# Performance work log

Measured on AMD Instinct MI355X. Metric: run time of the kernel, lower is better.

Reference implementation:

```python
import jax, jax.numpy as jnp
import numpy as np

EMBED_DIM = 512
NUM_HEADS = 8
HEAD_DIM = EMBED_DIM // NUM_HEADS
FACTOR = 5
B, T = 4, 2048


def setup_inputs() -> dict:
    key = jax.random.key(0)
    ks = jax.random.split(key, 10)
    s = EMBED_DIM ** -0.5
    hidden_states = jax.random.normal(ks[0], (B, T, EMBED_DIM), dtype=jnp.float32)
    log_L = int(np.ceil(np.log1p(T)))
    u_part = min(FACTOR * T * log_L, T)
    index_sample = jax.random.randint(ks[1], (u_part,), 0, T, dtype=jnp.int32)
    Wq = jax.random.normal(ks[2], (EMBED_DIM, EMBED_DIM), dtype=jnp.float32) * s
    bq = jnp.zeros((EMBED_DIM,), dtype=jnp.float32)
    Wk = jax.random.normal(ks[3], (EMBED_DIM, EMBED_DIM), dtype=jnp.float32) * s
    bk = jnp.zeros((EMBED_DIM,), dtype=jnp.float32)
    Wv = jax.random.normal(ks[4], (EMBED_DIM, EMBED_DIM), dtype=jnp.float32) * s
    bv = jnp.zeros((EMBED_DIM,), dtype=jnp.float32)
    Wo = jax.random.normal(ks[5], (EMBED_DIM, EMBED_DIM), dtype=jnp.float32) * s
    bo = jnp.zeros((EMBED_DIM,), dtype=jnp.float32)
    return {"hidden_states": hidden_states, "index_sample": index_sample,
            "Wq": Wq, "bq": bq, "Wk": Wk, "bk": bk, "Wv": Wv, "bv": bv,
            "Wo": Wo, "bo": bo}


def _split_heads(x, bsz, seqlen):
    # [B, T, E] -> [B*H, T, head_dim]
    return x.reshape(bsz, seqlen, NUM_HEADS, HEAD_DIM).transpose(0, 2, 1, 3).reshape(bsz * NUM_HEADS, seqlen, HEAD_DIM)


def reference(hidden_states, index_sample, Wq, bq, Wk, bk, Wv, bv, Wo, bo):
    bsz, tgt_len, embed_dim = hidden_states.shape
    scaling = HEAD_DIM ** -0.5
    q = (hidden_states @ Wq.T + bq) * scaling
    k = hidden_states @ Wk.T + bk
    v = hidden_states @ Wv.T + bv
    q = _split_heads(q, bsz, tgt_len)   # [BH, T, d]
    k = _split_heads(k, bsz, tgt_len)
    v = _split_heads(v, bsz, tgt_len)
    L_k = tgt_len
    log_q = int(np.ceil(np.log1p(tgt_len)))
    u = min(FACTOR * log_q, tgt_len)
    # random key sampling (indices precomputed, length u_part)
    k_sample = k[:, index_sample, :]                                  # [BH, u_part, d]
    qk_sample = jnp.einsum('bqd,bkd->bqk', q, k_sample)               # [BH, T, u_part]
    # sparsity measurement: max - mean over sampled keys (mean uses full L_k as in source)
    sparsity = qk_sample.max(axis=-1) - qk_sample.sum(axis=-1) / L_k  # [BH, T]
    top_idx = jax.lax.top_k(sparsity, u)[1]                           # [BH, u]
    q_reduce = jnp.take_along_axis(q, top_idx[:, :, None], axis=1)    # [BH, u, d]
    attn = jax.nn.softmax(jnp.einsum('bud,bkd->buk', q_reduce, k), axis=-1)  # [BH, u, L]
    attn_out = jnp.einsum('buk,bkd->bud', attn, v)                    # [BH, u, d]
    # encoder context: mean of values over time, scattered with active-query outputs
    context = jnp.broadcast_to(v.mean(axis=1, keepdims=True), v.shape)  # [BH, T, d]
    bh_idx = jnp.arange(bsz * NUM_HEADS)[:, None]
    context = context.at[bh_idx, top_idx].set(attn_out)
    out = context.reshape(bsz, NUM_HEADS, tgt_len, HEAD_DIM).transpose(0, 2, 1, 3).reshape(bsz, tgt_len, embed_dim)
    return out @ Wo.T + bo
```

## Files before the change

kernel.cpp:

```cpp
#include <hip/hip_runtime.h>
#include <hip/hip_bf16.h>
#include <math.h>

#define T_LEN 2048
#define EMB   512
#define NHEAD 8
#define HDIM  64
#define BHEADS 32
#define USEL  40

typedef __bf16 bf16v8 __attribute__((ext_vector_type(8)));
typedef _Float16 f16x8 __attribute__((ext_vector_type(8)));
typedef float f32x4 __attribute__((ext_vector_type(4)));
typedef unsigned short u16;

__device__ __forceinline__ void cvt4_hilo(const float4 f, uint2& ph, uint2& pl)
{
    __hip_bfloat16 h0 = __float2bfloat16(f.x);
    __hip_bfloat16 h1 = __float2bfloat16(f.y);
    __hip_bfloat16 h2 = __float2bfloat16(f.z);
    __hip_bfloat16 h3 = __float2bfloat16(f.w);
    __hip_bfloat16 l0 = __float2bfloat16(f.x - __bfloat162float(h0));
    __hip_bfloat16 l1 = __float2bfloat16(f.y - __bfloat162float(h1));
    __hip_bfloat16 l2 = __float2bfloat16(f.z - __bfloat162float(h2));
    __hip_bfloat16 l3 = __float2bfloat16(f.w - __bfloat162float(h3));
    ph.x = (unsigned)*(const u16*)&h0 | ((unsigned)*(const u16*)&h1 << 16);
    ph.y = (unsigned)*(const u16*)&h2 | ((unsigned)*(const u16*)&h3 << 16);
    pl.x = (unsigned)*(const u16*)&l0 | ((unsigned)*(const u16*)&l1 << 16);
    pl.y = (unsigned)*(const u16*)&l2 | ((unsigned)*(const u16*)&l3 << 16);
}

__device__ __forceinline__ void cvt4_hilo_h(const float4 f, uint2& ph, uint2& pl)
{
    _Float16 h0 = (_Float16)f.x;
    _Float16 h1 = (_Float16)f.y;
    _Float16 h2 = (_Float16)f.z;
    _Float16 h3 = (_Float16)f.w;
    _Float16 l0 = (_Float16)(f.x - (float)h0);
    _Float16 l1 = (_Float16)(f.y - (float)h1);
    _Float16 l2 = (_Float16)(f.z - (float)h2);
    _Float16 l3 = (_Float16)(f.w - (float)h3);
    ph.x = (unsigned)*(const u16*)&h0 | ((unsigned)*(const u16*)&h1 << 16);
    ph.y = (unsigned)*(const u16*)&h2 | ((unsigned)*(const u16*)&h3 << 16);
    pl.x = (unsigned)*(const u16*)&l0 | ((unsigned)*(const u16*)&l1 << 16);
    pl.y = (unsigned)*(const u16*)&l2 | ((unsigned)*(const u16*)&l3 << 16);
}

__global__ __launch_bounds__(256)
void pack_hilo_kernel(const float* __restrict__ X,
                      const float* __restrict__ Wq, const float* __restrict__ Wk,
                      const float* __restrict__ Wv,
                      u16* __restrict__ Xp, u16* __restrict__ Wp)
{
    alignas(16) __shared__ u16 th[4096];
    alignas(16) __shared__ u16 tl[4096];
    const int b = blockIdx.x, tid = threadIdx.x;

    const float* src; u16* dst;
    if (b < 1024) {
        int mt = b >> 4, kt = b & 15;
        src = X + (size_t)(mt * 128) * EMB + kt * 32;
        dst = Xp + (size_t)b * 8192;
    } else {
        int wdx = b - 1024;
        int z = wdx >> 6, nt = (wdx >> 4) & 3, kt = wdx & 15;
        const float* W = (z == 0) ? Wq : (z == 1) ? Wk : Wv;
        src = W + (size_t)(nt * 128) * EMB + kt * 32;
        dst = Wp + (size_t)wdx * 8192;
    }

    #pragma unroll
    for (int s = 0; s < 4; ++s) {
        int u = tid + 256 * s;
        int row = u >> 3, c4 = u & 7;
        float4 f = *(const float4*)&src[(size_t)row * EMB + c4 * 4];
        uint2 ph, pl;
        cvt4_hilo_h(f, ph, pl);
        int kq = c4 >> 1, e4 = (c4 & 1) * 4;
        *(uint2*)&th[kq * 1024 + row * 8 + e4] = ph;
        *(uint2*)&tl[kq * 1024 + row * 8 + e4] = pl;
    }
    __syncthreads();

    uint4* d4 = (uint4*)dst;
    const uint4* s4h = (const uint4*)th;
    const uint4* s4l = (const uint4*)tl;
    d4[tid]       = s4h[tid];
    d4[tid + 256] = s4h[tid + 256];
    d4[tid + 512] = s4l[tid];
    d4[tid + 768] = s4l[tid + 256];
}

__global__ __launch_bounds__(256)
void qkv_mfma_kernel(const u16* __restrict__ Xp, const u16* __restrict__ Wp,
                     const float* __restrict__ bq, const float* __restrict__ bk,
                     const float* __restrict__ bv,
                     float* __restrict__ qo, float* __restrict__ ko, float* __restrict__ vo)
{
    alignas(16) __shared__ u16 Ah[4096];
    alignas(16) __shared__ u16 Al[4096];
    alignas(16) __shared__ u16 Bh[4096];
    alignas(16) __shared__ u16 Bl[4096];

    const int z = blockIdx.z;
    const float* bias; float* dst; float scale;
    if (z == 0)      { bias = bq; dst = qo; scale = 0.125f; }
    else if (z == 1) { bias = bk; dst = ko; scale = 1.0f;   }
    else             { bias = bv; dst = vo; scale = 1.0f;   }
    const bool three = (z != 2);

    const int tid = threadIdx.x;
    const int mt = blockIdx.x;
    const int nt = blockIdx.y;
    const int w = tid >> 6, lane = tid & 63;
    const int wm = w & 1, wn = w >> 1;
    const int lm = lane & 15, kq = lane >> 4;

    const u16* Abase = Xp + (size_t)mt * (16 * 8192);
    const u16* Bbase = Wp + (size_t)(z * 4 + nt) * (16 * 8192);

    f32x4 acc[4][4];
    #pragma unroll
    for (int i = 0; i < 4; ++i)
        #pragma unroll
        for (int j = 0; j < 4; ++j)
            #pragma unroll
            for (int r = 0; r < 4; ++r) acc[i][j][r] = 0.0f;

    for (int kt = 0; kt < 16; ++kt) {
        __syncthreads();
        const u16* at = Abase + kt * 8192;
        const u16* bt = Bbase + kt * 8192;
        const u16* gsrc; u16* ldst;
        if (w == 0)      { gsrc = at;        ldst = Ah; }
        else if (w == 1) { gsrc = at + 4096; ldst = Al; }
        else if (w == 2) { gsrc = bt;        ldst = Bh; }
        else             { gsrc = bt + 4096; ldst = Bl; }
        if (three || (w & 1) == 0) {
            #pragma unroll
            for (int i = 0; i < 8; ++i)
                __builtin_amdgcn_global_load_lds(
                    (const __attribute__((address_space(1))) void*)(gsrc + (size_t)lane * 8 + i * 512),
                    (__attribute__((address_space(3))) void*)(ldst + i * 512),
                    16, 0, 0);
        }
        __syncthreads();

        f16x8 ah[4], al[4], bh[4], bl[4];
        #pragma unroll
        for (int i = 0; i < 4; ++i) {
            int ar = (wm * 64 + i * 16 + lm) * 8 + kq * 1024;
            int br = (wn * 64 + i * 16 + lm) * 8 + kq * 1024;
            ah[i] = *(const f16x8*)&Ah[ar];
            bh[i] = *(const f16x8*)&Bh[br];
            if (three) {
                al[i] = *(const f16x8*)&Al[ar];
                bl[i] = *(const f16x8*)&Bl[br];
            }
        }
        #pragma unroll
        for (int i = 0; i < 4; ++i)
            #pragma unroll
            for (int j = 0; j < 4; ++j) {
                acc[i][j] = __builtin_amdgcn_mfma_f32_16x16x32_f16(ah[i], bh[j], acc[i][j], 0, 0, 0);
                if (three) {
                    acc[i][j] = __builtin_amdgcn_mfma_f32_16x16x32_f16(ah[i], bl[j], acc[i][j], 0, 0, 0);
                    acc[i][j] = __builtin_amdgcn_mfma_f32_16x16x32_f16(al[i], bh[j], acc[i][j], 0, 0, 0);
                }
            }
    }

    #pragma unroll
    for (int j = 0; j < 4; ++j) {
        int ng = nt * 128 + wn * 64 + j * 16 + lm;
        int h = ng >> 6, d = ng & 63;
        float bv_ = bias[ng];
        #pragma unroll
        for (int i = 0; i < 4; ++i) {
            #pragma unroll
            for (int r = 0; r < 4; ++r) {
                int mg = mt * 128 + wm * 64 + i * 16 + kq * 4 + r;
                int b = mg >> 11, t = mg & 2047;
                dst[((size_t)((b * NHEAD + h) * T_LEN + t)) * HDIM + d] =
                    (acc[i][j][r] + bv_) * scale;
            }
        }
    }
}

__global__ __launch_bounds__(256)
void qkv_proj_kernel(const float* __restrict__ X,
                     const float* __restrict__ Wq, const float* __restrict__ bq,
                     const float* __restrict__ Wk, const float* __restrict__ bk,
                     const float* __restrict__ Wv, const float* __restrict__ bv,
                     float* __restrict__ qo, float* __restrict__ ko, float* __restrict__ vo)
{
    alignas(16) __shared__ u16 Ah[128 * 40];
    alignas(16) __shared__ u16 Al[128 * 40];
    alignas(16) __shared__ u16 Bh[128 * 40];
    alignas(16) __shared__ u16 Bl[128 * 40];

    const int z = blockIdx.z;
    const float* W; const float* bias; float* dst; float scale;
    if (z == 0)      { W = Wq; bias = bq; dst = qo; scale = 0.125f; }
    else if (z == 1) { W = Wk; bias = bk; dst = ko; scale = 1.0f;   }
    else             { W = Wv; bias = bv; dst = vo; scale = 1.0f;   }

    const int tid = threadIdx.x;
    const int m0 = blockIdx.x * 128;
    const int n0 = blockIdx.y * 128;
    const int w = tid >> 6, lane = tid & 63;
    const int wm = w & 1, wn = w >> 1;
    const int lm = lane & 15, kq = lane >> 4;

    f32x4 acc[4][4];
    #pragma unroll
    for (int i = 0; i < 4; ++i)
        #pragma unroll
        for (int j = 0; j < 4; ++j)
            #pragma unroll
            for (int r = 0; r < 4; ++r) acc[i][j][r] = 0.0f;

    for (int kc = 0; kc < EMB; kc += 32) {
        __syncthreads();
        #pragma unroll
        for (int s = 0; s < 4; ++s) {
            int u = tid + 256 * s;
            int row = u >> 3, c4 = u & 7;
            float4 fa = *(const float4*)&X[(size_t)(m0 + row) * EMB + kc + c4 * 4];
            float4 fb = *(const float4*)&W[(n0 + row) * EMB + kc + c4 * 4];
            uint2 ph, pl;
            cvt4_hilo_h(fa, ph, pl);
            *(uint2*)&Ah[row * 40 + c4 * 4] = ph;
            *(uint2*)&Al[row * 40 + c4 * 4] = pl;
            cvt4_hilo_h(fb, ph, pl);
            *(uint2*)&Bh[row * 40 + c4 * 4] = ph;
            *(uint2*)&Bl[row * 40 + c4 * 4] = pl;
        }
        __syncthreads();

        f16x8 ah[4], al[4], bh[4], bl[4];
        #pragma unroll
        for (int i = 0; i < 4; ++i) {
            int ra = (wm * 64 + i * 16 + lm) * 40 + kq * 8;
            ah[i] = *(const f16x8*)&Ah[ra];
            al[i] = *(const f16x8*)&Al[ra];
            int rb = (wn * 64 + i * 16 + lm) * 40 + kq * 8;
            bh[i] = *(const f16x8*)&Bh[rb];
            bl[i] = *(const f16x8*)&Bl[rb];
        }
        #pragma unroll
        for (int i = 0; i < 4; ++i)
            #pragma unroll
            for (int j = 0; j < 4; ++j) {
                acc[i][j] = __builtin_amdgcn_mfma_f32_16x16x32_f16(ah[i], bh[j], acc[i][j], 0, 0, 0);
                acc[i][j] = __builtin_amdgcn_mfma_f32_16x16x32_f16(ah[i], bl[j], acc[i][j], 0, 0, 0);
                acc[i][j] = __builtin_amdgcn_mfma_f32_16x16x32_f16(al[i], bh[j], acc[i][j], 0, 0, 0);
            }
    }

    #pragma unroll
    for (int j = 0; j < 4; ++j) {
        int ng = n0 + wn * 64 + j * 16 + lm;
        int h = ng >> 6, d = ng & 63;
        float bv_ = bias[ng];
        #pragma unroll
        for (int i = 0; i < 4; ++i) {
            #pragma unroll
            for (int r = 0; r < 4; ++r) {
                int mg = m0 + wm * 64 + i * 16 + kq * 4 + r;
                int b = mg >> 11, t = mg & 2047;
                dst[((size_t)((b * NHEAD + h) * T_LEN + t)) * HDIM + d] =
                    (acc[i][j][r] + bv_) * scale;
            }
        }
    }
}

__global__ __launch_bounds__(256)
void count_compact_kernel(const int* __restrict__ idxs, int n,
                          int* __restrict__ count, int* __restrict__ klist,
                          int* __restrict__ ncp)
{
    __shared__ int cnt[T_LEN];
    __shared__ int th_tot[256];
    __shared__ int th_off[256];
    __shared__ int ncs;
    const int tid = threadIdx.x;
    for (int j = tid; j < T_LEN; j += 256) cnt[j] = 0;
    __syncthreads();
    for (int i = tid; i < n; i += 256) atomicAdd(&cnt[idxs[i] & (T_LEN - 1)], 1);
    __syncthreads();
    const int base = tid * 8;
    int flags[8]; int loc = 0;
    #pragma unroll
    for (int j = 0; j < 8; ++j) {
        int c = cnt[base + j];
        count[base + j] = c;
        flags[j] = (c > 0); loc += flags[j];
    }
    th_tot[tid] = loc;
    __syncthreads();
    if (tid == 0) {
        int run = 0;
        for (int i = 0; i < 256; ++i) { th_off[i] = run; run += th_tot[i]; }
        ncs = run;
        ncp[0] = run;
    }
    __syncthreads();
    int off = th_off[tid];
    #pragma unroll
    for (int j = 0; j < 8; ++j)
        if (flags[j]) klist[off++] = base + j;
    __syncthreads();
    const int nc = ncs;
    const int nt = (nc + 127) & ~127;
    const int k0 = klist[0];
    for (int j = nc + tid; j < nt; j += 256) klist[j] = k0;
}

__global__ __launch_bounds__(256)
void ksum_vmean_part_kernel(const int* __restrict__ count,
                            const float* __restrict__ k, const float* __restrict__ v,
                            float* __restrict__ kpart, float* __restrict__ vpart)
{
    __shared__ int cs[256];
    alignas(16) __shared__ float rk[16 * 64];
    alignas(16) __shared__ float rv[16 * 64];

    const int sl = blockIdx.x, bh = blockIdx.y, tid = threadIdx.x;
    const int f4 = tid & 15, tg = tid >> 4;
    const int t0 = sl * 256;

    cs[tid] = count[t0 + tid];
    __syncthreads();

    const float4* k4 = (const float4*)(k + (size_t)bh * T_LEN * HDIM) + t0 * 16;
    const float4* v4 = (const float4*)(v + (size_t)bh * T_LEN * HDIM) + t0 * 16;

    float4 ak = {0.f, 0.f, 0.f, 0.f}, av = {0.f, 0.f, 0.f, 0.f};
    #pragma unroll
    for (int s = 0; s < 16; ++s) {
        int t = tg + s * 16;
        float c = (float)cs[t];
        float4 kf = k4[t * 16 + f4];
        float4 vf = v4[t * 16 + f4];
        ak.x = fmaf(c, kf.x, ak.x); ak.y = fmaf(c, kf.y, ak.y);
        ak.z = fmaf(c, kf.z, ak.z); ak.w = fmaf(c, kf.w, ak.w);
        av.x += vf.x; av.y += vf.y; av.z += vf.z; av.w += vf.w;
    }
    *(float4*)&rk[tg * 64 + f4 * 4] = ak;
    *(float4*)&rv[tg * 64 + f4 * 4] = av;
    __syncthreads();

    if (tid < 64) {
        float sk = 0.f, sv = 0.f;
        #pragma unroll
        for (int g = 0; g < 16; ++g) { sk += rk[g * 64 + tid]; sv += rv[g * 64 + tid]; }
        kpart[((size_t)bh * 8 + sl) * 64 + tid] = sk;
        vpart[((size_t)bh * 8 + sl) * 64 + tid] = sv;
    }
}

__global__ __launch_bounds__(64)
void ksum_vmean_reduce_kernel(const float* __restrict__ kpart, const float* __restrict__ vpart,
                              float* __restrict__ ksum, float* __restrict__ vmean)
{
    const int bh = blockIdx.x, d = threadIdx.x;
    float sk = 0.f, sv = 0.f;
    #pragma unroll
    for (int sl = 0; sl < 8; ++sl) {
        sk += kpart[((size_t)bh * 8 + sl) * 64 + d];
        sv += vpart[((size_t)bh * 8 + sl) * 64 + d];
    }
    ksum[bh * 64 + d]  = sk;
    vmean[bh * 64 + d] = sv * (1.0f / 2048.0f);
}

__global__ __launch_bounds__(256)
void pack_k_kernel(const float* __restrict__ k, const int* __restrict__ klist,
                   const int* __restrict__ ncp, u16* __restrict__ Kp)
{
    alignas(16) __shared__ u16 th[8192];
    alignas(16) __shared__ u16 tl[8192];
    const int wg = blockIdx.x, tid = threadIdx.x;
    const int swz = (wg & 7) * 64 + (wg >> 3);
    const int bh = swz >> 4, kt = swz & 15;
    const int ntiles = (ncp[0] + 127) >> 7;
    if (kt >= ntiles) return;

    const float4* kb4 = (const float4*)(k + (size_t)bh * T_LEN * HDIM);
    #pragma unroll
    for (int s = 0; s < 8; ++s) {
        int u = tid + 256 * s;
        int row = u >> 4, c4 = u & 15;
        int krow = klist[kt * 128 + row];
        float4 f = kb4[krow * 16 + c4];
        uint2 ph, pl;
        cvt4_hilo_h(f, ph, pl);
        int base = (c4 >> 3) * 4096 + ((c4 >> 1) & 3) * 1024 + row * 8 + (c4 & 1) * 4;
        *(uint2*)&th[base] = ph;
        *(uint2*)&tl[base] = pl;
    }
    __syncthreads();

    u16* dst = Kp + ((size_t)bh * 16 + kt) * 16384;
    uint4* d4 = (uint4*)dst;
    const uint4* s4h = (const uint4*)th;
    const uint4* s4l = (const uint4*)tl;
    #pragma unroll
    for (int i = 0; i < 4; ++i) d4[tid + 256 * i] = s4h[tid + 256 * i];
    #pragma unroll
    for (int i = 0; i < 4; ++i) d4[1024 + tid + 256 * i] = s4l[tid + 256 * i];
}

__global__ __launch_bounds__(256)
void sparsity_scan_kernel(const float* __restrict__ q, const u16* __restrict__ Kp,
                          const float* __restrict__ ksum,
                          const int* __restrict__ ncp, float* __restrict__ spars)
{
    alignas(16) __shared__ u16 KH[10240];
    alignas(16) __shared__ u16 KL[10240];
    __shared__ float ksm[64];
    __shared__ float smax[128];
    __shared__ float sdotL[128];

    const int tid = threadIdx.x;
    const int wg = blockIdx.x;
    const int swz = (wg & 7) * 64 + (wg >> 3);
    const int bh = swz >> 4;
    const int q0 = (swz & 15) * 128;
    const int w = tid >> 6, lane = tid & 63;
    const int lm = lane & 15, kq = lane >> 4;

    const float* qb = q + ((size_t)bh * T_LEN + q0) * HDIM;
    const int ntiles = (ncp[0] + 127) >> 7;

    if (tid < 64) ksm[tid] = ksum[bh * 64 + tid];

    #pragma unroll
    for (int s = 0; s < 8; ++s) {
        int u = tid + 256 * s;
        int row = u >> 4, c4 = u & 15;
        float4 f = *(const float4*)&qb[row * HDIM + c4 * 4];
        uint2 ph, pl;
        cvt4_hilo_h(f, ph, pl);
        int base = ((c4 >> 3) * 128 + row) * 40 + (c4 & 7) * 4;
        *(uint2*)&KH[base] = ph;
        *(uint2*)&KL[base] = pl;
    }
    __syncthreads();

    f16x8 qh[2][2], ql[2][2];
    #pragma unroll
    for (int i = 0; i < 2; ++i)
        #pragma unroll
        for (int c = 0; c < 2; ++c) {
            int ra = (c * 128 + w * 32 + i * 16 + lm) * 40 + kq * 8;
            qh[i][c] = *(const f16x8*)&KH[ra];
            ql[i][c] = *(const f16x8*)&KL[ra];
        }

    {
        float4 k0a = *(const float4*)&ksm[kq * 8];
        float4 k0b = *(const float4*)&ksm[kq * 8 + 4];
        float4 k1a = *(const float4*)&ksm[32 + kq * 8];
        float4 k1b = *(const float4*)&ksm[32 + kq * 8 + 4];
        float kmv[2][8] = {{k0a.x, k0a.y, k0a.z, k0a.w, k0b.x, k0b.y, k0b.z, k0b.w},
                           {k1a.x, k1a.y, k1a.z, k1a.w, k1b.x, k1b.y, k1b.z, k1b.w}};
        #pragma unroll
        for (int i = 0; i < 2; ++i) {
            float sd = 0.f;
            #pragma unroll
            for (int c = 0; c < 2; ++c)
                #pragma unroll
                for (int e = 0; e < 8; ++e)
                    sd = fmaf((float)qh[i][c][e] + (float)ql[i][c][e], kmv[c][e], sd);
            sd += __shfl_xor(sd, 16, 64);
            sd += __shfl_xor(sd, 32, 64);
            if (kq == 0) sdotL[w * 32 + i * 16 + lm] = sd;
        }
    }

    float vmax[2][4];
    #pragma unroll
    for (int i = 0; i < 2; ++i)
        #pragma unroll
        for (int r = 0; r < 4; ++r) vmax[i][r] = -INFINITY;

    const u16* kpb = Kp + (size_t)bh * (16 * 16384);

    for (int kt = 0; kt < ntiles; ++kt) {
        __syncthreads();
        const u16* kp = kpb + kt * 16384;
        const u16* gsrc; u16* ldst;
        if (w == 0)      { gsrc = kp;         ldst = KH; }
        else if (w == 1) { gsrc = kp + 4096;  ldst = KH + 4096; }
        else if (w == 2) { gsrc = kp + 8192;  ldst = KL; }
        else             { gsrc = kp + 12288; ldst = KL + 4096; }
        #pragma unroll
        for (int i = 0; i < 8; ++i)
            __builtin_amdgcn_global_load_lds(
                (const __attribute__((address_space(1))) void*)(gsrc + (size_t)lane * 8 + i * 512),
                (__attribute__((address_space(3))) void*)(ldst + i * 512),
                16, 0, 0);
        __syncthreads();

        #pragma unroll
        for (int j = 0; j < 8; ++j) {
            int rb0 = kq * 1024 + (j * 16 + lm) * 8;
            int rb1 = 4096 + kq * 1024 + (j * 16 + lm) * 8;
            f16x8 bh0 = *(const f16x8*)&KH[rb0];
            f16x8 bl0 = *(const f16x8*)&KL[rb0];
            f16x8 bh1 = *(const f16x8*)&KH[rb1];
            f16x8 bl1 = *(const f16x8*)&KL[rb1];
            f32x4 a0 = {0.f, 0.f, 0.f, 0.f};
            f32x4 a1 = {0.f, 0.f, 0.f, 0.f};
            a0 = __builtin_amdgcn_mfma_f32_16x16x32_f16(qh[0][0], bh0, a0, 0, 0, 0);
            a1 = __builtin_amdgcn_mfma_f32_16x16x32_f16(qh[1][0], bh0, a1, 0, 0, 0);
            a0 = __builtin_amdgcn_mfma_f32_16x16x32_f16(qh[0][0], bl0, a0, 0, 0, 0);
            a1 = __builtin_amdgcn_mfma_f32_16x16x32_f16(qh[1][0], bl0, a1, 0, 0, 0);
            a0 = __builtin_amdgcn_mfma_f32_16x16x32_f16(ql[0][0], bh0, a0, 0, 0, 0);
            a1 = __builtin_amdgcn_mfma_f32_16x16x32_f16(ql[1][0], bh0, a1, 0, 0, 0);
            a0 = __builtin_amdgcn_mfma_f32_16x16x32_f16(qh[0][1], bh1, a0, 0, 0, 0);
            a1 = __builtin_amdgcn_mfma_f32_16x16x32_f16(qh[1][1], bh1, a1, 0, 0, 0);
            a0 = __builtin_amdgcn_mfma_f32_16x16x32_f16(qh[0][1], bl1, a0, 0, 0, 0);
            a1 = __builtin_amdgcn_mfma_f32_16x16x32_f16(qh[1][1], bl1, a1, 0, 0, 0);
            a0 = __builtin_amdgcn_mfma_f32_16x16x32_f16(ql[0][1], bh1, a0, 0, 0, 0);
            a1 = __builtin_amdgcn_mfma_f32_16x16x32_f16(ql[1][1], bh1, a1, 0, 0, 0);
            #pragma unroll
            for (int r = 0; r < 4; ++r) {
                vmax[0][r] = fmaxf(vmax[0][r], a0[r]);
                vmax[1][r] = fmaxf(vmax[1][r], a1[r]);
            }
        }
    }

    #pragma unroll
    for (int i = 0; i < 2; ++i)
        #pragma unroll
        for (int r = 0; r < 4; ++r) {
            float m = vmax[i][r];
            m = fmaxf(m, __shfl_xor(m, 1, 64));
            m = fmaxf(m, __shfl_xor(m, 2, 64));
            m = fmaxf(m, __shfl_xor(m, 4, 64));
            m = fmaxf(m, __shfl_xor(m, 8, 64));
            if (lm == 0) smax[w * 32 + i * 16 + kq * 4 + r] = m;
        }
    __syncthreads();

    if (tid < 128)
        spars[bh * T_LEN + q0 + tid] = smax[tid] - sdotL[tid] * (1.0f / 2048.0f);
}

__global__ __launch_bounds__(256)
void sparsity_scan_fb_kernel(const float* __restrict__ q, const float* __restrict__ k,
                             const float* __restrict__ ksum, const int* __restrict__ klist,
                             const int* __restrict__ ncp, float* __restrict__ spars)
{
    alignas(16) __shared__ u16 KH[256 * 40];
    alignas(16) __shared__ u16 KL[256 * 40];
    __shared__ float ksm[64];
    __shared__ float smax[128];
    __shared__ float sdotL[128];

    const int tid = threadIdx.x;
    const int bh = blockIdx.y;
    const int q0 = blockIdx.x * 128;
    const int w = tid >> 6, lane = tid & 63;
    const int lm = lane & 15, kq = lane >> 4;

    const float* qb = q + ((size_t)bh * T_LEN + q0) * HDIM;
    const float4* kb4 = (const float4*)(k + (size_t)bh * T_LEN * HDIM);
    const int ntiles = (ncp[0] + 127) >> 7;

    if (tid < 64) ksm[tid] = ksum[bh * 64 + tid];

    #pragma unroll
    for (int s = 0; s < 8; ++s) {
        int u = tid + 256 * s;
        int row = u >> 4, c4 = u & 15;
        float4 f = *(const float4*)&qb[row * HDIM + c4 * 4];
        uint2 ph, pl;
        cvt4_hilo_h(f, ph, pl);
        int base = ((c4 >> 3) * 128 + row) * 40 + (c4 & 7) * 4;
        *(uint2*)&KH[base] = ph;
        *(uint2*)&KL[base] = pl;
    }
    __syncthreads();

    f16x8 qh[2][2], ql[2][2];
    #pragma unroll
    for (int i = 0; i < 2; ++i)
        #pragma unroll
        for (int c = 0; c < 2; ++c) {
            int ra = (c * 128 + w * 32 + i * 16 + lm) * 40 + kq * 8;
            qh[i][c] = *(const f16x8*)&KH[ra];
            ql[i][c] = *(const f16x8*)&KL[ra];
        }

    {
        float4 k0a = *(const float4*)&ksm[kq * 8];
        float4 k0b = *(const float4*)&ksm[kq * 8 + 4];
        float4 k1a = *(const float4*)&ksm[32 + kq * 8];
        float4 k1b = *(const float4*)&ksm[32 + kq * 8 + 4];
        float kmv[2][8] = {{k0a.x, k0a.y, k0a.z, k0a.w, k0b.x, k0b.y, k0b.z, k0b.w},
                           {k1a.x, k1a.y, k1a.z, k1a.w, k1b.x, k1b.y, k1b.z, k1b.w}};
        #pragma unroll
        for (int i = 0; i < 2; ++i) {
            float sd = 0.f;
            #pragma unroll
            for (int c = 0; c < 2; ++c)
                #pragma unroll
                for (int e = 0; e < 8; ++e)
                    sd = fmaf((float)qh[i][c][e] + (float)ql[i][c][e], kmv[c][e], sd);
            sd += __shfl_xor(sd, 16, 64);
            sd += __shfl_xor(sd, 32, 64);
            if (kq == 0) sdotL[w * 32 + i * 16 + lm] = sd;
        }
    }

    float vmax[2][4];
    #pragma unroll
    for (int i = 0; i < 2; ++i)
        #pragma unroll
        for (int r = 0; r < 4; ++r) vmax[i][r] = -INFINITY;

    for (int kt = 0; kt < ntiles; ++kt) {
        __syncthreads();
        #pragma unroll
        for (int s = 0; s < 8; ++s) {
            int u = tid + 256 * s;
            int row = u >> 4, c4 = u & 15;
            int krow = klist[kt * 128 + row];
            float4 f = kb4[krow * 16 + c4];
            uint2 ph, pl;
            cvt4_hilo_h(f, ph, pl);
            int base = ((c4 >> 3) * 128 + row) * 40 + (c4 & 7) * 4;
            *(uint2*)&KH[base] = ph;
            *(uint2*)&KL[base] = pl;
        }
        __syncthreads();

        #pragma unroll
        for (int j = 0; j < 8; ++j) {
            int rb0 = (j * 16 + lm) * 40 + kq * 8;
            int rb1 = (128 + j * 16 + lm) * 40 + kq * 8;
            f16x8 bh0 = *(const f16x8*)&KH[rb0];
            f16x8 bl0 = *(const f16x8*)&KL[rb0];
            f16x8 bh1 = *(const f16x8*)&KH[rb1];
            f16x8 bl1 = *(const f16x8*)&KL[rb1];
            f32x4 a0 = {0.f, 0.f, 0.f, 0.f};
            f32x4 a1 = {0.f, 0.f, 0.f, 0.f};
            a0 = __builtin_amdgcn_mfma_f32_16x16x32_f16(qh[0][0], bh0, a0, 0, 0, 0);
            a1 = __builtin_amdgcn_mfma_f32_16x16x32_f16(qh[1][0], bh0, a1, 0, 0, 0);
            a0 = __builtin_amdgcn_mfma_f32_16x16x32_f16(qh[0][0], bl0, a0, 0, 0, 0);
            a1 = __builtin_amdgcn_mfma_f32_16x16x32_f16(qh[1][0], bl0, a1, 0, 0, 0);
            a0 = __builtin_amdgcn_mfma_f32_16x16x32_f16(ql[0][0], bh0, a0, 0, 0, 0);
            a1 = __builtin_amdgcn_mfma_f32_16x16x32_f16(ql[1][0], bh0, a1, 0, 0, 0);
            a0 = __builtin_amdgcn_mfma_f32_16x16x32_f16(qh[0][1], bh1, a0, 0, 0, 0);
            a1 = __builtin_amdgcn_mfma_f32_16x16x32_f16(qh[1][1], bh1, a1, 0, 0, 0);
            a0 = __builtin_amdgcn_mfma_f32_16x16x32_f16(qh[0][1], bl1, a0, 0, 0, 0);
            a1 = __builtin_amdgcn_mfma_f32_16x16x32_f16(qh[1][1], bl1, a1, 0, 0, 0);
            a0 = __builtin_amdgcn_mfma_f32_16x16x32_f16(ql[0][1], bh1, a0, 0, 0, 0);
            a1 = __builtin_amdgcn_mfma_f32_16x16x32_f16(ql[1][1], bh1, a1, 0, 0, 0);
            #pragma unroll
            for (int r = 0; r < 4; ++r) {
                vmax[0][r] = fmaxf(vmax[0][r], a0[r]);
                vmax[1][r] = fmaxf(vmax[1][r], a1[r]);
            }
        }
    }

    #pragma unroll
    for (int i = 0; i < 2; ++i)
        #pragma unroll
        for (int r = 0; r < 4; ++r) {
            float m = vmax[i][r];
            m = fmaxf(m, __shfl_xor(m, 1, 64));
            m = fmaxf(m, __shfl_xor(m, 2, 64));
            m = fmaxf(m, __shfl_xor(m, 4, 64));
            m = fmaxf(m, __shfl_xor(m, 8, 64));
            if (lm == 0) smax[w * 32 + i * 16 + kq * 4 + r] = m;
        }
    __syncthreads();

    if (tid < 128)
        spars[bh * T_LEN + q0 + tid] = smax[tid] - sdotL[tid] * (1.0f / 2048.0f);
}

__global__ __launch_bounds__(256)
void topk_kernel(const float* __restrict__ spars, int* __restrict__ topi)
{
    __shared__ unsigned keys[T_LEN];
    __shared__ int hist[256];
    __shared__ int sfx[257];
    __shared__ int sh_need, sh_bin, nsel, neq, cnt2;
    const int bh = blockIdx.x, tid = threadIdx.x;

    #pragma unroll
    for (int s = 0; s < 8; ++s) {
        int j = tid + 256 * s;
        unsigned u = __float_as_uint(spars[bh * T_LEN + j]);
        keys[j] = (u & 0x80000000u) ? ~u : (u | 0x80000000u);
    }
    if (tid == 0) { sh_need = USEL; nsel = 0; neq = 0; cnt2 = 0; }
    __syncthreads();

    unsigned kpref = 0;
    int shift = 24;
    #pragma unroll
    for (int level = 0; level < 4; ++level) {
        const unsigned hi_mask = (shift == 24) ? 0u : (0xFFFFFFFFu << (shift + 8));
        hist[tid] = 0;
        __syncthreads();
        #pragma unroll
        for (int s = 0; s < 8; ++s) {
            unsigned kk = keys[tid + 256 * s];
            if ((kk & hi_mask) == kpref)
                atomicAdd(&hist[(kk >> shift) & 255], 1);
        }
        __syncthreads();
        sfx[tid] = hist[tid];
        if (tid == 0) sfx[256] = 0;
        __syncthreads();
        for (int off = 1; off < 256; off <<= 1) {
            int v = (tid + off < 256) ? sfx[tid + off] : 0;
            __syncthreads();
            sfx[tid] += v;
            __syncthreads();
        }
        const int need = sh_need;
        const int A = (tid == 255) ? 0 : sfx[tid + 1];
        const int here = sfx[tid];
        __syncthreads();
        if (A < need && here >= need) {
            sh_bin = tid;
            sh_need = need - A;
        }
        __syncthreads();
        kpref |= (unsigned)sh_bin << shift;
        shift -= 8;
    }

    const unsigned K = kpref;
    const int need_eq = sh_need;

    #pragma unroll
    for (int s = 0; s < 8; ++s) {
        int j = tid + 256 * s;
        unsigned kk = keys[j];
        if (kk > K) {
            int pos = atomicAdd(&nsel, 1);
            if (pos < USEL) topi[bh * USEL + pos] = j;
        } else if (kk == K) {
            atomicAdd(&neq, 1);
        }
    }
    __syncthreads();
    const int base = nsel;
    const int E = neq;
    __syncthreads();

    if (E == need_eq) {
        #pragma unroll
        for (int s = 0; s < 8; ++s) {
            int j = tid + 256 * s;
            if (keys[j] == K) {
                int pos = atomicAdd(&cnt2, 1);
                if (base + pos < USEL) topi[bh * USEL + base + pos] = j;
            }
        }
    } else {
        #pragma unroll
        for (int s = 0; s < 8; ++s) {
            int j = tid + 256 * s;
            if (keys[j] == K) {
                int rank = 0;
                for (int j2 = 0; j2 < j; ++j2) rank += (keys[j2] == K);
                if (rank < need_eq && base + rank < USEL)
                    topi[bh * USEL + base + rank] = j;
            }
        }
    }
}

__global__ __launch_bounds__(256)
void gather_q_kernel(const float* __restrict__ q, const int* __restrict__ topi,
                     float* __restrict__ qsel)
{
    const int bh = blockIdx.x, tid = threadIdx.x;
    for (int i = tid; i < USEL * HDIM; i += 256) {
        int u = i >> 6, d = i & 63;
        int t = topi[bh * USEL + u] & (T_LEN - 1);
        qsel[(size_t)bh * USEL * HDIM + i] = q[((size_t)bh * T_LEN + t) * HDIM + d];
    }
}

__global__ __launch_bounds__(256)
void sel_scores_kernel(const float* __restrict__ qsel, const float* __restrict__ k,
                       float* __restrict__ S)
{
    __shared__ float qsT[64 * 41];
    __shared__ float ksT[64 * 257];

    const int sl = blockIdx.x, bh = blockIdx.y, tid = threadIdx.x;
    const int t0 = sl * 256;

    for (int i = tid; i < USEL * HDIM; i += 256) {
        int u = i >> 6, d = i & 63;
        qsT[d * 41 + u] = qsel[(size_t)bh * USEL * HDIM + i];
    }
    const float4* k4 = (const float4*)(k + (size_t)bh * T_LEN * HDIM);
    #pragma unroll
    for (int s = 0; s < 16; ++s) {
        int u = tid + 256 * s;
        int c4 = u & 15, t = u >> 4;
        float4 f = k4[(t0 + t) * 16 + c4];
        ksT[(c4 * 4 + 0) * 257 + t] = f.x;
        ksT[(c4 * 4 + 1) * 257 + t] = f.y;
        ksT[(c4 * 4 + 2) * 257 + t] = f.z;
        ksT[(c4 * 4 + 3) * 257 + t] = f.w;
    }
    __syncthreads();

    const int qg = tid >> 5;
    const int kg = tid & 31;

    float acc[5][8];
    #pragma unroll
    for (int i = 0; i < 5; ++i)
        #pragma unroll
        for (int j = 0; j < 8; ++j) acc[i][j] = 0.0f;

    #pragma unroll 4
    for (int d = 0; d < 64; ++d) {
        float qv[5], kv[8];
        #pragma unroll
        for (int i = 0; i < 5; ++i) qv[i] = qsT[d * 41 + qg * 5 + i];
        #pragma unroll
        for (int j = 0; j < 8; ++j) kv[j] = ksT[d * 257 + kg + 32 * j];
        #pragma unroll
        for (int i = 0; i < 5; ++i)
            #pragma unroll
            for (int j = 0; j < 8; ++j)
                acc[i][j] = fmaf(qv[i], kv[j], acc[i][j]);
    }

    #pragma unroll
    for (int i = 0; i < 5; ++i) {
        float* sp = &S[((size_t)bh * USEL + qg * 5 + i) * T_LEN + t0 + kg];
        #pragma unroll
        for (int j = 0; j < 8; ++j) sp[32 * j] = acc[i][j];
    }
}

__global__ __launch_bounds__(256)
void sel_softmax_kernel(float* __restrict__ S)
{
    __shared__ float red[256];
    const int row = blockIdx.x, tid = threadIdx.x;
    float* sr = S + (size_t)row * T_LEN;

    float x[8];
    float m = -INFINITY;
    #pragma unroll
    for (int s = 0; s < 8; ++s) { x[s] = sr[tid + 256 * s]; m = fmaxf(m, x[s]); }
    red[tid] = m;
    __syncthreads();
    for (int s = 128; s > 0; s >>= 1) {
        if (tid < s) red[tid] = fmaxf(red[tid], red[tid + s]);
        __syncthreads();
    }
    m = red[0];
    __syncthreads();

    float sum = 0.f;
    #pragma unroll
    for (int s = 0; s < 8; ++s) { x[s] = __expf(x[s] - m); sum += x[s]; }
    red[tid] = sum;
    __syncthreads();
    for (int s = 128; s > 0; s >>= 1) {
        if (tid < s) red[tid] += red[tid + s];
        __syncthreads();
    }
    float inv = 1.0f / red[0];
    #pragma unroll
    for (int s = 0; s < 8; ++s) sr[tid + 256 * s] = x[s] * inv;
}

__global__ __launch_bounds__(256)
void pv_part_kernel(const float* __restrict__ S, const float* __restrict__ v,
                    float* __restrict__ part)
{
    __shared__ float ps[USEL * 128];
    __shared__ float vs[128 * 69];
    __shared__ float obuf[128 * 20];

    const int sl = blockIdx.x, bh = blockIdx.y, tid = threadIdx.x;
    const int t0 = sl * 128;

    for (int i = tid; i < USEL * 128; i += 256) {
        int q = i >> 7, t = i & 127;
        ps[q * 128 + t] = S[((size_t)bh * USEL + q) * T_LEN + t0 + t];
    }
    const float4* v4 = (const float4*)(v + (size_t)bh * T_LEN * HDIM);
    #pragma unroll
    for (int s = 0; s < 8; ++s) {
        int u = tid + 256 * s;
        int c4 = u & 15, t = u >> 4;
        float4 f = v4[(t0 + t) * 16 + c4];
        vs[t * 69 + c4 * 4 + 0] = f.x;
        vs[t * 69 + c4 * 4 + 1] = f.y;
        vs[t * 69 + c4 * 4 + 2] = f.z;
        vs[t * 69 + c4 * 4 + 3] = f.w;
    }
    __syncthreads();

    const int qg = tid >> 5, r = tid & 31;
    const int dg = r >> 1, th = r & 1;
    const int tb = th * 64;

    float o[5][4];
    #pragma unroll
    for (int i = 0; i < 5; ++i)
        #pragma unroll
        for (int j = 0; j < 4; ++j) o[i][j] = 0.0f;

    #pragma unroll 4
    for (int tt = 0; tt < 64; ++tt) {
        int t = tb + tt;
        float pv[5];
        #pragma unroll
        for (int i = 0; i < 5; ++i) pv[i] = ps[(qg * 5 + i) * 128 + t];
        float4 vv = *(const float4*)&vs[t * 69 + dg * 4];
        #pragma unroll
        for (int i = 0; i < 5; ++i) {
            o[i][0] = fmaf(pv[i], vv.x, o[i][0]);
            o[i][1] = fmaf(pv[i], vv.y, o[i][1]);
            o[i][2] = fmaf(pv[i], vv.z, o[i][2]);
            o[i][3] = fmaf(pv[i], vv.w, o[i][3]);
        }
    }

    const int p = qg * 16 + dg;
    if (th == 1) {
        #pragma unroll
        for (int i = 0; i < 5; ++i)
            #pragma unroll
            for (int j = 0; j < 4; ++j) obuf[p * 20 + i * 4 + j] = o[i][j];
    }
    __syncthreads();
    if (th == 0) {
        float* pb = part + ((size_t)bh * 16 + sl) * (USEL * HDIM);
        #pragma unroll
        for (int i = 0; i < 5; ++i)
            #pragma unroll
            for (int j = 0; j < 4; ++j)
                pb[(qg * 5 + i) * HDIM + dg * 4 + j] = o[i][j] + obuf[p * 20 + i * 4 + j];
    }
}

__global__ __launch_bounds__(256)
void pv_merge_kernel(const float* __restrict__ part, float* __restrict__ attn)
{
    const int bh = blockIdx.x, tid = threadIdx.x;
    for (int i = tid; i < USEL * HDIM; i += 256) {
        float s = 0.f;
        #pragma unroll
        for (int sl = 0; sl < 16; ++sl)
            s += part[((size_t)bh * 16 + sl) * (USEL * HDIM) + i];
        attn[(size_t)bh * USEL * HDIM + i] = s;
    }
}

__global__ __launch_bounds__(256)
void ctx_fill_kernel(const float* __restrict__ vmean, float* __restrict__ ctx)
{
    int flat = blockIdx.x * 256 + threadIdx.x;
    int d = flat & 63, h = (flat >> 6) & 7, b = flat >> 20;
    int bh = (b << 3) | h;
    ctx[flat] = vmean[bh * 64 + d];
}

__global__ void ctx_scatter_kernel(const float* __restrict__ attn, const int* __restrict__ topi,
                                   float* __restrict__ ctx)
{
    const int u = blockIdx.x, bh = blockIdx.y, d = threadIdx.x;
    const int b = bh >> 3, h = bh & 7;
    const int t = topi[bh * USEL + u] & (T_LEN - 1);
    ctx[(size_t)(b * T_LEN + t) * EMB + h * 64 + d] =
        attn[((size_t)bh * USEL + u) * HDIM + d];
}

__global__ __launch_bounds__(256)
void out_proj_kernel(const float* __restrict__ A, const float* __restrict__ Wo,
                     const float* __restrict__ bo, float* __restrict__ out)
{
    alignas(16) __shared__ u16 Ah[128 * 40];
    alignas(16) __shared__ u16 Al[128 * 40];
    alignas(16) __shared__ u16 Bh[128 * 40];
    alignas(16) __shared__ u16 Bl[128 * 40];

    const int tid = threadIdx.x;
    const int m0 = blockIdx.x * 128;
    const int n0 = blockIdx.y * 128;
    const int w = tid >> 6, lane = tid & 63;
    const int wm = w & 1, wn = w >> 1;
    const int lm = lane & 15, kq = lane >> 4;

    f32x4 acc[4][4];
    #pragma unroll
    for (int i = 0; i < 4; ++i)
        #pragma unroll
        for (int j = 0; j < 4; ++j)
            #pragma unroll
            for (int r = 0; r < 4; ++r) acc[i][j][r] = 0.0f;

    for (int kc = 0; kc < EMB; kc += 32) {
        __syncthreads();
        #pragma unroll
        for (int s = 0; s < 4; ++s) {
            int u = tid + 256 * s;
            int row = u >> 3, c4 = u & 7;
            float4 fa = *(const float4*)&A[(size_t)(m0 + row) * EMB + kc + c4 * 4];
            float4 fb = *(const float4*)&Wo[(n0 + row) * EMB + kc + c4 * 4];
            uint2 ph, pl;
            cvt4_hilo(fa, ph, pl);
            *(uint2*)&Ah[row * 40 + c4 * 4] = ph;
            *(uint2*)&Al[row * 40 + c4 * 4] = pl;
            cvt4_hilo(fb, ph, pl);
            *(uint2*)&Bh[row * 40 + c4 * 4] = ph;
            *(uint2*)&Bl[row * 40 + c4 * 4] = pl;
        }
        __syncthreads();

        bf16v8 ah[4], al[4], bh[4], bl[4];
        #pragma unroll
        for (int i = 0; i < 4; ++i) {
            int ra = (wm * 64 + i * 16 + lm) * 40 + kq * 8;
            ah[i] = *(const bf16v8*)&Ah[ra];
            al[i] = *(const bf16v8*)&Al[ra];
            int rb = (wn * 64 + i * 16 + lm) * 40 + kq * 8;
            bh[i] = *(const bf16v8*)&Bh[rb];
            bl[i] = *(const bf16v8*)&Bl[rb];
        }
        #pragma unroll
        for (int i = 0; i < 4; ++i)
            #pragma unroll
            for (int j = 0; j < 4; ++j) {
                acc[i][j] = __builtin_amdgcn_mfma_f32_16x16x32_bf16(ah[i], bh[j], acc[i][j], 0, 0, 0);
                acc[i][j] = __builtin_amdgcn_mfma_f32_16x16x32_bf16(ah[i], bl[j], acc[i][j], 0, 0, 0);
                acc[i][j] = __builtin_amdgcn_mfma_f32_16x16x32_bf16(al[i], bh[j], acc[i][j], 0, 0, 0);
            }
    }

    #pragma unroll
    for (int j = 0; j < 4; ++j) {
        int ng = n0 + wn * 64 + j * 16 + lm;
        float bias = bo[ng];
        #pragma unroll
        for (int i = 0; i < 4; ++i)
            #pragma unroll
            for (int r = 0; r < 4; ++r) {
                int mg = m0 + wm * 64 + i * 16 + kq * 4 + r;
                out[(size_t)mg * EMB + ng] = acc[i][j][r] + bias;
            }
    }
}

__global__ __launch_bounds__(256)
void ws_diag_kernel(float* __restrict__ out, int n, float mib)
{
    int flat = blockIdx.x * 256 + threadIdx.x;
    if (flat < n) out[flat] = mib;
}

extern "C" void kernel_launch(void* const* d_in, const int* in_sizes, int n_in,
                              void* d_out, int out_size, void* d_ws, size_t ws_size,
                              hipStream_t stream)
{
    const float* X = nullptr; const int* idxs = nullptr;
    const float* Wseen[4] = {nullptr, nullptr, nullptr, nullptr};
    const float* bseen[4] = {nullptr, nullptr, nullptr, nullptr};
    int nw = 0, nb = 0, u_part = 2048;
    for (int i = 0; i < n_in; ++i) {
        int sz = in_sizes[i];
        if (sz == EMB * EMB * 16) { if (!X) X = (const float*)d_in[i]; }
        else if (sz == T_LEN)     { if (!idxs) { idxs = (const int*)d_in[i]; u_part = sz; } }
        else if (sz == EMB * EMB) { if (nw < 4) Wseen[nw++] = (const float*)d_in[i]; }
        else if (sz == EMB)       { if (nb < 4) bseen[nb++] = (const float*)d_in[i]; }
    }
    if (!X || !idxs || nw < 4 || nb < 4) {
        X = (const float*)d_in[0]; idxs = (const int*)d_in[1];
        Wseen[0] = (const float*)d_in[2]; bseen[0] = (const float*)d_in[3];
        Wseen[1] = (const float*)d_in[4]; bseen[1] = (const float*)d_in[5];
        Wseen[2] = (const float*)d_in[6]; bseen[2] = (const float*)d_in[7];
        Wseen[3] = (const float*)d_in[8]; bseen[3] = (const float*)d_in[9];
        u_part = in_sizes[1];
    }
    const float *Wq = Wseen[0], *Wk = Wseen[1], *Wv = Wseen[2], *Wo = Wseen[3];
    const float *bq = bseen[0], *bk = bseen[1], *bv = bseen[2], *bo = bseen[3];

    const size_t NEED      = 50951168ULL;
    const size_t NEED_BIG  = NEED + 16777216ULL + 3145728ULL;
    if (ws_size < NEED) {
        ws_diag_kernel<<<(out_size + 255) / 256, 256, 0, stream>>>(
            (float*)d_out, out_size, (float)(ws_size >> 20));
        return;
    }

    float* ws    = (float*)d_ws;
    float* qw    = ws;
    float* kw    = qw + 4194304;
    float* vw    = kw + 4194304;
    float* tail  = vw + 4194304;
    float* slotA = tail;
    float* spars = tail + 81920;
    int*   count = (int*)(tail + 147456);
    float* ksum  = tail + 149504;
    float* vmean = tail + 151552;
    int*   topi  = (int*)(tail + 153600);
    float* kpart = tail;
    float* vpart = tail + 16384;
    int*   klist = (int*)(tail + 32768);
    int*   ncp   = (int*)(tail + 34816);
    float* S     = qw;
    float* pvp   = qw + 2621440;
    float* qsel  = slotA;
    float* attn  = slotA;
    float* ctx   = (float*)d_ws;
    u16*   Xp    = (u16*)((char*)d_ws + NEED);
    u16*   Wp    = Xp + 8388608;
    u16*   Kp    = Xp;

    const bool big = (ws_size >= NEED_BIG);

    if (big) {
        pack_hilo_kernel<<<1216, 256, 0, stream>>>(X, Wq, Wk, Wv, Xp, Wp);
        qkv_mfma_kernel<<<dim3(64, 4, 3), 256, 0, stream>>>(Xp, Wp, bq, bk, bv, qw, kw, vw);
    } else {
        qkv_proj_kernel<<<dim3(64, 4, 3), 256, 0, stream>>>(X, Wq, bq, Wk, bk, Wv, bv, qw, kw, vw);
    }
    count_compact_kernel<<<1, 256, 0, stream>>>(idxs, u_part, count, klist, ncp);
    ksum_vmean_part_kernel<<<dim3(8, 32), 256, 0, stream>>>(count, kw, vw, kpart, vpart);
    ksum_vmean_reduce_kernel<<<32, 64, 0, stream>>>(kpart, vpart, ksum, vmean);
    if (big) {
        pack_k_kernel<<<512, 256, 0, stream>>>(kw, klist, ncp, Kp);
        sparsity_scan_kernel<<<512, 256, 0, stream>>>(qw, Kp, ksum, ncp, spars);
    } else {
        sparsity_scan_fb_kernel<<<dim3(16, 32), 256, 0, stream>>>(qw, kw, ksum, klist, ncp, spars);
    }
    topk_kernel<<<32, 256, 0, stream>>>(spars, topi);
    gather_q_kernel<<<32, 256, 0, stream>>>(qw, topi, qsel);
    sel_scores_kernel<<<dim3(8, 32), 256, 0, stream>>>(qsel, kw, S);
    sel_softmax_kernel<<<1280, 256, 0, stream>>>(S);
    pv_part_kernel<<<dim3(16, 32), 256, 0, stream>>>(S, vw, pvp);
    pv_merge_kernel<<<32, 256, 0, stream>>>(pvp, attn);
    ctx_fill_kernel<<<16384, 256, 0, stream>>>(vmean, ctx);
    ctx_scatter_kernel<<<dim3(USEL, BHEADS), 64, 0, stream>>>(attn, topi, ctx);
    out_proj_kernel<<<dim3(64, 4), 256, 0, stream>>>(ctx, Wo, bo, (float*)d_out);
}
```

Measured before the change: 280.0 us.

## Double-buffer LDS tiles in QKV MFMA GEMM to overlap loads with compute

```diff
diff --git a/kernel.cpp b/kernel.cpp
--- a/kernel.cpp
+++ b/kernel.cpp
@@ -97,10 +97,10 @@
                      const float* __restrict__ bv,
                      float* __restrict__ qo, float* __restrict__ ko, float* __restrict__ vo)
 {
-    alignas(16) __shared__ u16 Ah[4096];
-    alignas(16) __shared__ u16 Al[4096];
-    alignas(16) __shared__ u16 Bh[4096];
-    alignas(16) __shared__ u16 Bl[4096];
+    alignas(16) __shared__ u16 Ah[2][4096];
+    alignas(16) __shared__ u16 Al[2][4096];
+    alignas(16) __shared__ u16 Bh[2][4096];
+    alignas(16) __shared__ u16 Bl[2][4096];
 
     const int z = blockIdx.z;
     const float* bias; float* dst; float scale;
@@ -127,15 +127,14 @@
             #pragma unroll
             for (int r = 0; r < 4; ++r) acc[i][j][r] = 0.0f;
 
-    for (int kt = 0; kt < 16; ++kt) {
-        __syncthreads();
+    auto stage = [&](int kt, int buf) {
         const u16* at = Abase + kt * 8192;
         const u16* bt = Bbase + kt * 8192;
         const u16* gsrc; u16* ldst;
-        if (w == 0)      { gsrc = at;        ldst = Ah; }
-        else if (w == 1) { gsrc = at + 4096; ldst = Al; }
-        else if (w == 2) { gsrc = bt;        ldst = Bh; }
-        else             { gsrc = bt + 4096; ldst = Bl; }
+        if (w == 0)      { gsrc = at;        ldst = &Ah[buf][0]; }
+        else if (w == 1) { gsrc = at + 4096; ldst = &Al[buf][0]; }
+        else if (w == 2) { gsrc = bt;        ldst = &Bh[buf][0]; }
+        else             { gsrc = bt + 4096; ldst = &Bl[buf][0]; }
         if (three || (w & 1) == 0) {
             #pragma unroll
             for (int i = 0; i < 8; ++i)
@@ -144,18 +143,31 @@
                     (__attribute__((address_space(3))) void*)(ldst + i * 512),
                     16, 0, 0);
         }
-        __syncthreads();
+    };
+
+    stage(0, 0);
+
+    for (int kt = 0; kt < 16; ++kt) {
+        const int cur = kt & 1;
+        if (kt + 1 < 16) {
+            stage(kt + 1, cur ^ 1);
+            asm volatile("s_waitcnt vmcnt(8)" ::: "memory");
+        } else {
+            asm volatile("s_waitcnt vmcnt(0)" ::: "memory");
+        }
+        __builtin_amdgcn_s_barrier();
+        __builtin_amdgcn_sched_barrier(0);
 
         f16x8 ah[4], al[4], bh[4], bl[4];
         #pragma unroll
         for (int i = 0; i < 4; ++i) {
             int ar = (wm * 64 + i * 16 + lm) * 8 + kq * 1024;
             int br = (wn * 64 + i * 16 + lm) * 8 + kq * 1024;
-            ah[i] = *(const f16x8*)&Ah[ar];
-            bh[i] = *(const f16x8*)&Bh[br];
+            ah[i] = *(const f16x8*)&Ah[cur][ar];
+            bh[i] = *(const f16x8*)&Bh[cur][br];
             if (three) {
-                al[i] = *(const f16x8*)&Al[ar];
-                bl[i] = *(const f16x8*)&Bl[br];
+                al[i] = *(const f16x8*)&Al[cur][ar];
+                bl[i] = *(const f16x8*)&Bl[cur][br];
             }
         }
         #pragma unroll
@@ -168,6 +180,7 @@
                     acc[i][j] = __builtin_amdgcn_mfma_f32_16x16x32_f16(al[i], bh[j], acc[i][j], 0, 0, 0);
                 }
             }
+        __builtin_amdgcn_s_barrier();
     }
 
     #pragma unroll
```

Result: no change. 277.0 us (-1.1%).
